# Kernel optimization log

Hardware: AMD Instinct MI355X
Metric: run time of the kernel (lower is better)

## Reference

```python
import jax, jax.numpy as jnp
import numpy as np

B, S, I, H = 128, 256, 512, 512


def setup_inputs() -> dict:
    key = jax.random.key(0)
    ks = jax.random.split(key, 7)
    scale = 1.0 / np.sqrt(H)
    return {
        "x": jax.random.normal(ks[0], (B, S, I), dtype=jnp.float32),
        "hx": jax.random.normal(ks[1], (B, H), dtype=jnp.float32),
        "mask": jax.random.uniform(ks[2], (B, S, 1), dtype=jnp.float32),
        # torch nn.GRUCell params: weight_ih [3H, I], weight_hh [3H, H], biases [3H]
        "W_ih": jax.random.uniform(ks[3], (3 * H, I), minval=-scale, maxval=scale, dtype=jnp.float32),
        "W_hh": jax.random.uniform(ks[4], (3 * H, H), minval=-scale, maxval=scale, dtype=jnp.float32),
        "b_ih": jax.random.uniform(ks[5], (3 * H,), minval=-scale, maxval=scale, dtype=jnp.float32),
        "b_hh": jax.random.uniform(ks[6], (3 * H,), minval=-scale, maxval=scale, dtype=jnp.float32),
    }


def reference(x, hx, mask, W_ih, W_hh, b_ih, b_hh):
    # Precompute input projections for all timesteps in one big GEMM: [B,S,3H]
    gi = jnp.einsum("bsi,gi->bsg", x, W_ih) + b_ih
    gi_s = jnp.moveaxis(gi, 1, 0)      # [S,B,3H]
    mask_s = jnp.moveaxis(mask, 1, 0)  # [S,B,1]

    def step(h, inp):
        gi_t, m_t = inp
        h = h * m_t                                    # masked reset of hidden state
        gh = h @ W_hh.T + b_hh                         # [B,3H]
        i_r, i_z, i_n = jnp.split(gi_t, 3, axis=-1)    # torch gate order: r, z, n
        h_r, h_z, h_n = jnp.split(gh, 3, axis=-1)
        r = jax.nn.sigmoid(i_r + h_r)
        z = jax.nn.sigmoid(i_z + h_z)
        n = jnp.tanh(i_n + r * h_n)
        h_new = (1.0 - z) * n + z * h
        return h_new, h_new

    h_last, hs = jax.lax.scan(step, hx, (gi_s, mask_s))
    return jnp.moveaxis(hs, 0, 1), h_last  # ([B,S,H], [B,H])
```

## Files before the change

### kernel.cpp

```cpp
#include <hip/hip_runtime.h>

typedef __attribute__((ext_vector_type(8))) short bf16x8;
typedef __attribute__((ext_vector_type(4))) float f32x4;
typedef unsigned short ushort_t;
typedef unsigned int uint32;

#define DEVI __device__ __forceinline__

static constexpr int Bn = 128, Sn = 256, In = 512, Hn = 512;
static constexpr int G3 = 3 * Hn;
static constexpr int GBLK = 32;

static constexpr size_t GI_OFF    = 0;
static constexpr size_t GI_BYTES  = (size_t)Bn * Sn * G3 * 2;
static constexpr size_t WIH_OFF   = GI_OFF + GI_BYTES;
static constexpr size_t WIH_BYTES = (size_t)G3 * In * 2;
static constexpr size_t HBUF_OFF  = WIH_OFF + WIH_BYTES;
static constexpr size_t HBUF_BYTES= (size_t)2 * Bn * Hn * 2;
static constexpr size_t BAR_OFF   = HBUF_OFF + HBUF_BYTES;

DEVI ushort_t f2bf(float f) {
  uint32 u = __builtin_bit_cast(uint32, f);
  u += 0x7FFFu + ((u >> 16) & 1u);
  return (ushort_t)(u >> 16);
}
DEVI float bf2f(ushort_t h) {
  uint32 u = ((uint32)h) << 16;
  return __builtin_bit_cast(float, u);
}
DEVI float sigmoid_f(float x) { return 1.0f / (1.0f + __expf(-x)); }
DEVI float tanh_f(float x)    { return 2.0f / (1.0f + __expf(-2.0f * x)) - 1.0f; }

DEVI void gbar(uint32* bar, uint32 target) {
  __syncthreads();
  if (threadIdx.x == 0) {
    __threadfence();
    __hip_atomic_fetch_add(bar, 1u, __ATOMIC_RELAXED, __HIP_MEMORY_SCOPE_AGENT);
    for (int spin = 0; spin < 1000000; ++spin) {
      if (__hip_atomic_load(bar, __ATOMIC_RELAXED, __HIP_MEMORY_SCOPE_AGENT) >= target)
        break;
      __builtin_amdgcn_s_sleep(1);
    }
    __threadfence();
  }
  __syncthreads();
}

__global__ void k_cvt_wih(const float* __restrict__ wih, ushort_t* __restrict__ out) {
  int i = blockIdx.x * blockDim.x + threadIdx.x;
  const float4 v = ((const float4*)wih)[i];
  ushort4 o;
  o.x = f2bf(v.x); o.y = f2bf(v.y); o.z = f2bf(v.z); o.w = f2bf(v.w);
  ((ushort4*)out)[i] = o;
}

__launch_bounds__(512)
__global__ void k_gi(const float* __restrict__ x, const ushort_t* __restrict__ wihb,
                     const float* __restrict__ b_ih, ushort_t* __restrict__ gi) {
  extern __shared__ ushort_t apan[];
  const int tid = threadIdx.x;
  const int bm  = blockIdx.x;
#pragma unroll
  for (int it = 0; it < 32; ++it) {
    int fidx = it * 512 + tid;
    int row = fidx >> 7, c4 = fidx & 127;
    const float4 v = *(const float4*)(x + ((size_t)(bm * 128 + row) << 9) + (c4 << 2));
    ushort4 o;
    o.x = f2bf(v.x); o.y = f2bf(v.y); o.z = f2bf(v.z); o.w = f2bf(v.w);
    *(ushort4*)(&apan[row * 520 + (c4 << 2)]) = o;
  }
  __syncthreads();
  const int lane = tid & 63, wid = tid >> 6;
  const int l15 = lane & 15, hi = lane >> 4;
  const int arow = wid * 16 + l15;
  for (int nt = 0; nt < 12; ++nt) {
    const int n0 = nt * 128;
    f32x4 acc[8] = {};
#pragma unroll
    for (int ks = 0; ks < 16; ++ks) {
      bf16x8 a = *(const bf16x8*)(&apan[arow * 520 + ks * 32 + hi * 8]);
#pragma unroll
      for (int j = 0; j < 8; ++j) {
        const ushort_t* wp = wihb + ((size_t)(n0 + j * 16 + l15) << 9) + ks * 32 + hi * 8;
        bf16x8 b = *(const bf16x8*)wp;
        acc[j] = __builtin_amdgcn_mfma_f32_16x16x32_bf16(a, b, acc[j], 0, 0, 0);
      }
    }
#pragma unroll
    for (int j = 0; j < 8; ++j) {
      const int n = n0 + j * 16 + l15;
      const float bias = b_ih[n];
#pragma unroll
      for (int r = 0; r < 4; ++r) {
        int m = bm * 128 + wid * 16 + hi * 4 + r;
        gi[(size_t)m * 1536 + n] = f2bf(acc[j][r] + bias);
      }
    }
  }
}

__launch_bounds__(512)
__global__ void k_scan(const float* __restrict__ hx, const float* __restrict__ mask,
                       const float* __restrict__ whh, const float* __restrict__ bhh,
                       const ushort_t* __restrict__ gi, ushort_t* __restrict__ hbuf,
                       uint32* __restrict__ bar, float* __restrict__ out) {
  __shared__ ushort_t Wl[48 * 520];
  __shared__ float hown[128 * 16];
  const int tid = threadIdx.x;
  const int c0 = blockIdx.x * 16;

  for (int r = 0; r < 48; ++r) {
    int g = r >> 4, j = r & 15;
    Wl[r * 520 + tid] = f2bf(whh[(size_t)(g * 512 + c0 + j) * 512 + tid]);
  }
  for (int i = tid; i < 2048; i += 512) {
    int b = i >> 4, j = i & 15;
    float v = hx[b * 512 + c0 + j] * mask[b * 256];
    hown[b * 16 + j] = v;
    hbuf[b * 512 + c0 + j] = f2bf(v);
  }
  uint32 tgt = GBLK;
  gbar(bar, tgt);

  const int lane = tid & 63, wid = tid >> 6;
  const int l15 = lane & 15, hi = lane >> 4;
  const float bhh_r = bhh[c0 + l15];
  const float bhh_z = bhh[512 + c0 + l15];
  const float bhh_n = bhh[1024 + c0 + l15];
  const int arow = wid * 16 + l15;
  int p = 0;

  for (int t = 0; t < 256; ++t) {
    float giv0[4], giv1[4], giv2[4], mk[4];
#pragma unroll
    for (int r = 0; r < 4; ++r) {
      int b = wid * 16 + hi * 4 + r;
      size_t gb = (size_t)(b * 256 + t) * 1536 + c0 + l15;
      giv0[r] = bf2f(gi[gb]);
      giv1[r] = bf2f(gi[gb + 512]);
      giv2[r] = bf2f(gi[gb + 1024]);
      mk[r] = (t < 255) ? mask[b * 256 + t + 1] : 0.0f;
    }

    const ushort_t* hb = hbuf + (size_t)p * (128 * 512);
    f32x4 acc[3] = {};
#pragma unroll
    for (int ks = 0; ks < 16; ++ks) {
      bf16x8 a = *(const bf16x8*)(hb + arow * 512 + ks * 32 + hi * 8);
#pragma unroll
      for (int g = 0; g < 3; ++g) {
        bf16x8 w = *(const bf16x8*)(&Wl[(g * 16 + l15) * 520 + ks * 32 + hi * 8]);
        acc[g] = __builtin_amdgcn_mfma_f32_16x16x32_bf16(a, w, acc[g], 0, 0, 0);
      }
    }

    ushort_t* hw = hbuf + (size_t)(p ^ 1) * (128 * 512);
#pragma unroll
    for (int r = 0; r < 4; ++r) {
      int b = wid * 16 + hi * 4 + r;
      float rg = sigmoid_f(giv0[r] + acc[0][r] + bhh_r);
      float zg = sigmoid_f(giv1[r] + acc[1][r] + bhh_z);
      float ng = tanh_f(giv2[r] + rg * (acc[2][r] + bhh_n));
      float hin = hown[b * 16 + l15];
      float hn = (1.0f - zg) * ng + zg * hin;
      out[(size_t)(b * 256 + t) * 512 + c0 + l15] = hn;
      if (t == 255) {
        out[(size_t)(128 * 256) * 512 + b * 512 + c0 + l15] = hn;
      } else {
        float hm = hn * mk[r];
        hown[b * 16 + l15] = hm;
        hw[b * 512 + c0 + l15] = f2bf(hm);
      }
    }
    if (t < 255) { tgt += GBLK; gbar(bar, tgt); p ^= 1; }
  }
}

extern "C" void kernel_launch(void* const* d_in, const int* in_sizes, int n_in,
                              void* d_out, int out_size, void* d_ws, size_t ws_size,
                              hipStream_t stream) {
  (void)in_sizes; (void)n_in; (void)out_size; (void)ws_size;
  const float* x    = (const float*)d_in[0];
  const float* hx   = (const float*)d_in[1];
  const float* mask = (const float*)d_in[2];
  const float* Wih  = (const float*)d_in[3];
  const float* Whh  = (const float*)d_in[4];
  const float* bih  = (const float*)d_in[5];
  const float* bhh  = (const float*)d_in[6];
  float* out = (float*)d_out;
  char* ws = (char*)d_ws;
  ushort_t* gi   = (ushort_t*)(ws + GI_OFF);
  ushort_t* wihb = (ushort_t*)(ws + WIH_OFF);
  ushort_t* hbuf = (ushort_t*)(ws + HBUF_OFF);
  uint32*   bar  = (uint32*)(ws + BAR_OFF);

  hipMemsetAsync(bar, 0, 256, stream);
  k_cvt_wih<<<768, 256, 0, stream>>>(Wih, wihb);
  k_gi<<<256, 512, 128 * 520 * 2, stream>>>(x, wihb, bih, gi);
  k_scan<<<GBLK, 512, 0, stream>>>(hx, mask, Whh, bhh, gi, hbuf, bar, out);
}
```

Before: 2.806 ms.

## Replace atomic-counter grid barrier with per-block flag barrier and atomic h exchange

The single shared atomic counter barrier is replaced by per-block flags on separate cache lines. Each block stores its step number to its own flag, and 32 threads poll all flags in parallel. Hidden-state exchange now goes through agent-scope relaxed 64-bit atomic stores and loads, which bypass stale caches without a full threadfence. The block's own h is kept in registers instead of LDS. The aim is to cut per-step barrier latency across the 256 sequential steps. The cost is relaxed ordering without explicit fences, plus a timeout abort path that could silently skip synchronisation.

```diff
diff --git a/kernel.cpp b/kernel.cpp
--- a/kernel.cpp
+++ b/kernel.cpp
@@ -4,6 +4,7 @@
 typedef __attribute__((ext_vector_type(4))) float f32x4;
 typedef unsigned short ushort_t;
 typedef unsigned int uint32;
+typedef unsigned long long u64;
 
 #define DEVI __device__ __forceinline__
 
@@ -17,7 +18,8 @@
 static constexpr size_t WIH_BYTES = (size_t)G3 * In * 2;
 static constexpr size_t HBUF_OFF  = WIH_OFF + WIH_BYTES;
 static constexpr size_t HBUF_BYTES= (size_t)2 * Bn * Hn * 2;
-static constexpr size_t BAR_OFF   = HBUF_OFF + HBUF_BYTES;
+static constexpr size_t FLAG_OFF  = HBUF_OFF + HBUF_BYTES;
+static constexpr size_t FLAG_BYTES= 4096;
 
 DEVI ushort_t f2bf(float f) {
   uint32 u = __builtin_bit_cast(uint32, f);
@@ -31,17 +33,21 @@
 DEVI float sigmoid_f(float x) { return 1.0f / (1.0f + __expf(-x)); }
 DEVI float tanh_f(float x)    { return 2.0f / (1.0f + __expf(-2.0f * x)) - 1.0f; }
 
-DEVI void gbar(uint32* bar, uint32 target) {
-  __syncthreads();
-  if (threadIdx.x == 0) {
-    __threadfence();
-    __hip_atomic_fetch_add(bar, 1u, __ATOMIC_RELAXED, __HIP_MEMORY_SCOPE_AGENT);
-    for (int spin = 0; spin < 1000000; ++spin) {
-      if (__hip_atomic_load(bar, __ATOMIC_RELAXED, __HIP_MEMORY_SCOPE_AGENT) >= target)
-        break;
-      __builtin_amdgcn_s_sleep(1);
-    }
-    __threadfence();
+DEVI void gbar2(uint32* flags, int bid, int tid, uint32 want, int* s_abort) {
+  __syncthreads();
+  if (*s_abort == 0) {
+    if (tid == 0)
+      __hip_atomic_store(flags + bid * 32, want, __ATOMIC_RELAXED,
+                         __HIP_MEMORY_SCOPE_AGENT);
+    if (tid < 32) {
+      int ok = 0;
+      for (int spin = 0; spin < 50000; ++spin) {
+        if (__hip_atomic_load(flags + tid * 32, __ATOMIC_RELAXED,
+                              __HIP_MEMORY_SCOPE_AGENT) >= want) { ok = 1; break; }
+        __builtin_amdgcn_s_sleep(1);
+      }
+      if (!ok) *s_abort = 1;
+    }
   }
   __syncthreads();
 }
@@ -102,32 +108,44 @@
 __launch_bounds__(512)
 __global__ void k_scan(const float* __restrict__ hx, const float* __restrict__ mask,
                        const float* __restrict__ whh, const float* __restrict__ bhh,
-                       const ushort_t* __restrict__ gi, ushort_t* __restrict__ hbuf,
-                       uint32* __restrict__ bar, float* __restrict__ out) {
+                       const ushort_t* __restrict__ gi, u64* __restrict__ hbuf,
+                       uint32* __restrict__ flags, float* __restrict__ out) {
   __shared__ ushort_t Wl[48 * 520];
-  __shared__ float hown[128 * 16];
+  __shared__ ushort_t hpack[128 * 16];
+  __shared__ int s_abort;
   const int tid = threadIdx.x;
-  const int c0 = blockIdx.x * 16;
+  const int bid = blockIdx.x;
+  const int c0 = bid * 16;
+  if (tid == 0) s_abort = 0;
 
   for (int r = 0; r < 48; ++r) {
     int g = r >> 4, j = r & 15;
     Wl[r * 520 + tid] = f2bf(whh[(size_t)(g * 512 + c0 + j) * 512 + tid]);
   }
-  for (int i = tid; i < 2048; i += 512) {
-    int b = i >> 4, j = i & 15;
-    float v = hx[b * 512 + c0 + j] * mask[b * 256];
-    hown[b * 16 + j] = v;
-    hbuf[b * 512 + c0 + j] = f2bf(v);
-  }
-  uint32 tgt = GBLK;
-  gbar(bar, tgt);
 
   const int lane = tid & 63, wid = tid >> 6;
   const int l15 = lane & 15, hi = lane >> 4;
+  const int arow = wid * 16 + l15;
+
+  float hreg[4];
+#pragma unroll
+  for (int r = 0; r < 4; ++r) {
+    int b = wid * 16 + hi * 4 + r;
+    hreg[r] = hx[b * 512 + c0 + l15] * mask[b * 256];
+    hpack[b * 16 + l15] = f2bf(hreg[r]);
+  }
+  __syncthreads();
+  {
+    int b = tid >> 2, q = tid & 3;
+    u64 v = *(const u64*)(&hpack[b * 16 + q * 4]);
+    __hip_atomic_store(hbuf + (size_t)b * 128 + (c0 >> 2) + q, v,
+                       __ATOMIC_RELAXED, __HIP_MEMORY_SCOPE_AGENT);
+  }
+  gbar2(flags, bid, tid, 1u, &s_abort);
+
   const float bhh_r = bhh[c0 + l15];
   const float bhh_z = bhh[512 + c0 + l15];
   const float bhh_n = bhh[1024 + c0 + l15];
-  const int arow = wid * 16 + l15;
   int p = 0;
 
   for (int t = 0; t < 256; ++t) {
@@ -142,37 +160,55 @@
       mk[r] = (t < 255) ? mask[b * 256 + t + 1] : 0.0f;
     }
 
-    const ushort_t* hb = hbuf + (size_t)p * (128 * 512);
+    const u64* hb = hbuf + (size_t)p * (128 * 128);
+    u64 a0[16], a1[16];
+#pragma unroll
+    for (int ks = 0; ks < 16; ++ks) {
+      size_t base = (size_t)arow * 128 + ks * 8 + hi * 2;
+      a0[ks] = __hip_atomic_load(hb + base, __ATOMIC_RELAXED, __HIP_MEMORY_SCOPE_AGENT);
+      a1[ks] = __hip_atomic_load(hb + base + 1, __ATOMIC_RELAXED, __HIP_MEMORY_SCOPE_AGENT);
+    }
+
     f32x4 acc[3] = {};
 #pragma unroll
     for (int ks = 0; ks < 16; ++ks) {
-      bf16x8 a = *(const bf16x8*)(hb + arow * 512 + ks * 32 + hi * 8);
+      union { u64 q[2]; bf16x8 v; } ua;
+      ua.q[0] = a0[ks]; ua.q[1] = a1[ks];
 #pragma unroll
       for (int g = 0; g < 3; ++g) {
         bf16x8 w = *(const bf16x8*)(&Wl[(g * 16 + l15) * 520 + ks * 32 + hi * 8]);
-        acc[g] = __builtin_amdgcn_mfma_f32_16x16x32_bf16(a, w, acc[g], 0, 0, 0);
-      }
-    }
-
-    ushort_t* hw = hbuf + (size_t)(p ^ 1) * (128 * 512);
+        acc[g] = __builtin_amdgcn_mfma_f32_16x16x32_bf16(ua.v, w, acc[g], 0, 0, 0);
+      }
+    }
+
 #pragma unroll
     for (int r = 0; r < 4; ++r) {
       int b = wid * 16 + hi * 4 + r;
       float rg = sigmoid_f(giv0[r] + acc[0][r] + bhh_r);
       float zg = sigmoid_f(giv1[r] + acc[1][r] + bhh_z);
       float ng = tanh_f(giv2[r] + rg * (acc[2][r] + bhh_n));
-      float hin = hown[b * 16 + l15];
-      float hn = (1.0f - zg) * ng + zg * hin;
+      float hn = (1.0f - zg) * ng + zg * hreg[r];
       out[(size_t)(b * 256 + t) * 512 + c0 + l15] = hn;
       if (t == 255) {
         out[(size_t)(128 * 256) * 512 + b * 512 + c0 + l15] = hn;
       } else {
         float hm = hn * mk[r];
-        hown[b * 16 + l15] = hm;
-        hw[b * 512 + c0 + l15] = f2bf(hm);
-      }
-    }
-    if (t < 255) { tgt += GBLK; gbar(bar, tgt); p ^= 1; }
+        hreg[r] = hm;
+        hpack[b * 16 + l15] = f2bf(hm);
+      }
+    }
+
+    if (t < 255) {
+      __syncthreads();
+      {
+        int b = tid >> 2, q = tid & 3;
+        u64 v = *(const u64*)(&hpack[b * 16 + q * 4]);
+        __hip_atomic_store(hbuf + (size_t)(p ^ 1) * (128 * 128) + (size_t)b * 128 + (c0 >> 2) + q,
+                           v, __ATOMIC_RELAXED, __HIP_MEMORY_SCOPE_AGENT);
+      }
+      gbar2(flags, bid, tid, (uint32)(t + 2), &s_abort);
+      p ^= 1;
+    }
   }
 }
 
@@ -189,13 +225,13 @@
   const float* bhh  = (const float*)d_in[6];
   float* out = (float*)d_out;
   char* ws = (char*)d_ws;
-  ushort_t* gi   = (ushort_t*)(ws + GI_OFF);
-  ushort_t* wihb = (ushort_t*)(ws + WIH_OFF);
-  ushort_t* hbuf = (ushort_t*)(ws + HBUF_OFF);
-  uint32*   bar  = (uint32*)(ws + BAR_OFF);
-
-  hipMemsetAsync(bar, 0, 256, stream);
+  ushort_t* gi    = (ushort_t*)(ws + GI_OFF);
+  ushort_t* wihb  = (ushort_t*)(ws + WIH_OFF);
+  u64*      hbuf  = (u64*)(ws + HBUF_OFF);
+  uint32*   flags = (uint32*)(ws + FLAG_OFF);
+
+  hipMemsetAsync(flags, 0, FLAG_BYTES, stream);
   k_cvt_wih<<<768, 256, 0, stream>>>(Wih, wihb);
   k_gi<<<256, 512, 128 * 520 * 2, stream>>>(x, wihb, bih, gi);
-  k_scan<<<GBLK, 512, 0, stream>>>(hx, mask, Whh, bhh, gi, hbuf, bar, out);
-}
+  k_scan<<<GBLK, 512, 0, stream>>>(hx, mask, Whh, bhh, gi, hbuf, flags, out);
+}
```

Measured after the change: 2.907 ms. 1.04x slower.
